# Performance work log

Measured on AMD Instinct MI355X. Metric: run time of the kernel, lower is better.

Reference implementation:

```python
import jax, jax.numpy as jnp
import numpy as np

SLOT_DIM = 128
HIDDEN = 64


def setup_inputs() -> dict:
    key = jax.random.key(0)
    k1, k2, k3, k4, k5 = jax.random.split(key, 5)
    b, k, d, h = 64, 128, SLOT_DIM, HIDDEN
    slots = jax.random.normal(k1, (b, k, d), dtype=jnp.float32)
    # edge_mlp params: Linear(2d -> h), Linear(h -> 1)
    s1 = 1.0 / np.sqrt(2 * d)
    W1 = jax.random.uniform(k2, (h, 2 * d), minval=-s1, maxval=s1, dtype=jnp.float32)
    b1 = jax.random.uniform(k3, (h,), minval=-s1, maxval=s1, dtype=jnp.float32)
    s2 = 1.0 / np.sqrt(h)
    W2 = jax.random.uniform(k4, (h,), minval=-s2, maxval=s2, dtype=jnp.float32)
    b2 = jax.random.uniform(k5, (), minval=-s2, maxval=s2, dtype=jnp.float32)
    return {"slots": slots, "W1": W1, "b1": b1, "W2": W2, "b2": b2}


def reference(slots, W1, b1, W2, b2):
    # slots: (b,k,d). Original concatenates [left,right] along features then
    # applies Linear(2d->h). Equivalent (same math): split W1 into halves and
    # broadcast-add, avoiding the (b,k,k,2d) concat tensor.
    b, k, d = slots.shape
    left_h = jnp.einsum('bkd,hd->bkh', slots, W1[:, :d])   # (b,k,h)
    right_h = jnp.einsum('bkd,hd->bkh', slots, W1[:, d:])  # (b,k,h)
    hidden = jax.nn.relu(left_h[:, :, None, :] + right_h[:, None, :, :] + b1)  # (b,k,k,h)
    logits = jnp.einsum('bijh,h->bij', hidden, W2) + b2    # (b,k,k)
    adj = jax.nn.sigmoid(logits)
    eye = jnp.eye(k, dtype=adj.dtype)[None]
    return adj * (1.0 - eye)
```

## Files before the change

kernel.cpp:

```cpp
#include <hip/hip_runtime.h>

#define BB 64
#define KK 128
#define DD 128

typedef __attribute__((ext_vector_type(8))) short bf16x8;
typedef __attribute__((ext_vector_type(4))) float f32x4;
typedef _Float16 half2v __attribute__((ext_vector_type(2)));
typedef __fp16 fp16x2 __attribute__((ext_vector_type(2)));

__device__ __forceinline__ unsigned cvt_pk_bf16(float x, float y) {
    unsigned r;
    asm("v_cvt_pk_bf16_f32 %0, %1, %2" : "=v"(r) : "v"(x), "v"(y));
    return r;
}

__device__ __forceinline__ unsigned cvt_pkrtz_u(float x, float y) {
    const fp16x2 pk = __builtin_amdgcn_cvt_pkrtz(x, y);
    return __builtin_bit_cast(unsigned, pk);
}

__device__ __forceinline__ unsigned pk_add_relu(unsigned a, unsigned b) {
    unsigned s, r;
    asm("v_pk_add_f16 %0, %1, %2" : "=v"(s) : "v"(a), "v"(b));
    asm("v_pk_max_f16 %0, %1, 0" : "=v"(r) : "v"(s));
    return r;
}

__device__ __forceinline__ float dot2acc(unsigned a, unsigned b, float c) {
#if __has_builtin(__builtin_amdgcn_fdot2)
    return __builtin_amdgcn_fdot2(__builtin_bit_cast(half2v, a),
                                  __builtin_bit_cast(half2v, b), c, false);
#else
    float r;
    asm("v_dot2_f32_f16 %0, %1, %2, %3" : "=v"(r) : "v"(a), "v"(b), "v"(c));
    return r;
#endif
}

__global__ __launch_bounds__(256, 2) void fused_kernel(
    const float* __restrict__ slots, const float* __restrict__ W1,
    const float* __restrict__ b1, const float* __restrict__ W2,
    const float* __restrict__ b2p, float* __restrict__ out)
{
    __shared__ unsigned smem_w[9632];
    char* smem = (char*)smem_w;

    const int t   = threadIdx.x;
    const int blk = blockIdx.x;
    const int b   = blk >> 3;
    const int it  = (blk >> 2) & 1;
    const int jt  = blk & 3;

    const int lane = t & 63;
    const int w    = t >> 6;
    const int lr   = lane & 15;
    const int lk   = lane >> 4;
    const int side = w >> 1;
    const int grp  = w & 1;

    const float b2 = *b2p;
    const float b1lo = (side == 0) ? b1[grp * 32 + lr]      : 0.0f;
    const float b1hi = (side == 0) ? b1[grp * 32 + 16 + lr] : 0.0f;
    float w2lo = 0.f, w2hi = 0.f;
    if (t < 32) {
        const int hl = (t & 15) + 32 * (t >> 4);
        w2lo = W2[hl]; w2hi = W2[hl + 16];
    }

    bf16x8 bfr[2][4];
#pragma unroll
    for (int n = 0; n < 2; ++n)
#pragma unroll
        for (int kf = 0; kf < 4; ++kf) {
            const int rowB = grp * 32 + n * 16 + lr;
            const float* p = W1 + rowB * 256 + side * 128 + kf * 32 + lk * 8;
            const float4 f0 = *reinterpret_cast<const float4*>(p);
            const float4 f1 = *reinterpret_cast<const float4*>(p + 4);
            uint4 pk;
            pk.x = cvt_pk_bf16(f0.x, f0.y); pk.y = cvt_pk_bf16(f0.z, f0.w);
            pk.z = cvt_pk_bf16(f1.x, f1.y); pk.w = cvt_pk_bf16(f1.z, f1.w);
            bfr[n][kf] = __builtin_bit_cast(bf16x8, pk);
        }

    {
        const float* srcI = slots + ((size_t)(b * KK) + it * 64) * DD;
        const float* srcJ = slots + ((size_t)(b * KK) + jt * 32) * DD;
#pragma unroll
        for (int x0 = 0; x0 < 1536; x0 += 256) {
            const int x = x0 + t;
            const int row = x >> 4, cb = x & 15;
            const float* src = (row < 64 ? srcI + row * DD
                                         : srcJ + (row - 64) * DD) + cb * 8;
            const float4 f0 = *reinterpret_cast<const float4*>(src);
            const float4 f1 = *reinterpret_cast<const float4*>(src + 4);
            uint4 pk;
            pk.x = cvt_pk_bf16(f0.x, f0.y); pk.y = cvt_pk_bf16(f0.z, f0.w);
            pk.z = cvt_pk_bf16(f1.x, f1.y); pk.w = cvt_pk_bf16(f1.z, f1.w);
            *reinterpret_cast<uint4*>(smem + row * 256 + ((cb ^ (row & 7)) << 4)) = pk;
        }
    }
    __syncthreads();

    f32x4 acc[4][2];
#pragma unroll
    for (int m = 0; m < 4; ++m)
#pragma unroll
        for (int n = 0; n < 2; ++n) acc[m][n] = f32x4{0.f, 0.f, 0.f, 0.f};

#pragma unroll
    for (int m = 0; m < 4; ++m) {
        if (side == 1 && m >= 2) continue;
#pragma unroll
        for (int kf = 0; kf < 4; ++kf) {
            const int row = side * 64 + 16 * m + lr;
            const int cb  = kf * 4 + lk;
            const bf16x8 af = *reinterpret_cast<const bf16x8*>(
                smem + row * 256 + ((cb ^ (row & 7)) << 4));
#pragma unroll
            for (int n = 0; n < 2; ++n)
                acc[m][n] = __builtin_amdgcn_mfma_f32_16x16x32_bf16(
                    af, bfr[n][kf], acc[m][n], 0, 0, 0);
        }
    }

    {
        unsigned* dst = smem_w + (side ? 8448 : 6144);
#pragma unroll
        for (int m = 0; m < 4; ++m) {
            if (side == 1 && m >= 2) continue;
#pragma unroll
            for (int r = 0; r < 4; ++r) {
                const int row = 16 * m + 4 * lk + r;
                dst[row * 36 + grp * 16 + lr] =
                    cvt_pkrtz_u(acc[m][0][r] + b1lo, acc[m][1][r] + b1hi);
            }
        }
        if (t < 32) smem_w[9600 + t] = cvt_pkrtz_u(w2lo, w2hi);
    }
    __syncthreads();

    const int tx = t & 15;
    const int ty = t >> 4;
    const unsigned* LsP = smem_w + 6144;
    const unsigned* RsP = smem_w + 8448;
    const unsigned* W2p = smem_w + 9600;

    uint4 w2r[8];
#pragma unroll
    for (int s = 0; s < 8; ++s)
        w2r[s] = *reinterpret_cast<const uint4*>(W2p + s * 4);

    float pacc[4][2] = {};
    uint4 l4a[4], r4a[2], l4b[4], r4b[2];

#define LD_STEP(L4, R4, s)                                                        \
    {                                                                             \
        _Pragma("unroll") for (int ii = 0; ii < 4; ++ii)                          \
            L4[ii] = *reinterpret_cast<const uint4*>(LsP + (ty + 16 * ii) * 36 + (s) * 4); \
        _Pragma("unroll") for (int jj = 0; jj < 2; ++jj)                          \
            R4[jj] = *reinterpret_cast<const uint4*>(RsP + (tx + 16 * jj) * 36 + (s) * 4); \
    }

#define COMPUTE_STEP(L4, R4, s)                                                   \
    {                                                                             \
        _Pragma("unroll") for (int ii = 0; ii < 4; ++ii)                          \
        _Pragma("unroll") for (int jj = 0; jj < 2; ++jj) {                        \
            float a = pacc[ii][jj];                                               \
            a = dot2acc(pk_add_relu(L4[ii].x, R4[jj].x), w2r[s].x, a);            \
            a = dot2acc(pk_add_relu(L4[ii].y, R4[jj].y), w2r[s].y, a);            \
            a = dot2acc(pk_add_relu(L4[ii].z, R4[jj].z), w2r[s].z, a);            \
            a = dot2acc(pk_add_relu(L4[ii].w, R4[jj].w), w2r[s].w, a);            \
            pacc[ii][jj] = a;                                                     \
        }                                                                         \
    }

    LD_STEP(l4a, r4a, 0)
#pragma unroll
    for (int sp = 0; sp < 4; ++sp) {
        LD_STEP(l4b, r4b, 2 * sp + 1)
        COMPUTE_STEP(l4a, r4a, 2 * sp)
        if (sp < 3) LD_STEP(l4a, r4a, 2 * sp + 2)
        COMPUTE_STEP(l4b, r4b, 2 * sp + 1)
    }
#undef LD_STEP
#undef COMPUTE_STEP

#pragma unroll
    for (int ii = 0; ii < 4; ++ii) {
        const int gi = it * 64 + ty + 16 * ii;
        float* orow = out + ((size_t)(b * KK) + gi) * KK + jt * 32;
#pragma unroll
        for (int jj = 0; jj < 2; ++jj) {
            const int jl = tx + 16 * jj;
            const int gj = jt * 32 + jl;
            const float xv = pacc[ii][jj] + b2;
            const float sg = 1.0f / (1.0f + __expf(-xv));
            orow[jl] = (gi == gj) ? 0.0f : sg;
        }
    }
}

extern "C" void kernel_launch(void* const* d_in, const int* in_sizes, int n_in,
                              void* d_out, int out_size, void* d_ws, size_t ws_size,
                              hipStream_t stream) {
    const float* slots = (const float*)d_in[0];
    const float* W1    = (const float*)d_in[1];
    const float* b1    = (const float*)d_in[2];
    const float* W2    = (const float*)d_in[3];
    const float* b2    = (const float*)d_in[4];
    float* out = (float*)d_out;
    (void)d_ws; (void)ws_size; (void)in_sizes; (void)n_in; (void)out_size;

    fused_kernel<<<BB * 8, 256, 0, stream>>>(slots, W1, b1, W2, b2, out);
}
```

Before: 14.88 us.

## Use 64x64 output tiles, load MFMA operands directly from global, remap blocks per XCD

Output tiles per block grow from 64x32 to 64x64, halving the grid to 256 blocks and cutting the redundant per-block first-layer GEMM work relative to pairwise output. The slot rows are no longer staged through swizzled shared memory. Each wave loads and converts its A fragments straight from global memory, which removes a barrier and shrinks LDS use. Block indices are remapped so that the blocks of one batch land on the same XCD for L2 locality. In exchange, fewer blocks than CUs may leave parts of the GPU idle, and the pairwise stage needs more registers per thread.

```diff
diff --git a/kernel.cpp b/kernel.cpp
--- a/kernel.cpp
+++ b/kernel.cpp
@@ -38,19 +38,20 @@
 #endif
 }
 
-__global__ __launch_bounds__(256, 2) void fused_kernel(
+__global__ __launch_bounds__(256) void fused_kernel(
     const float* __restrict__ slots, const float* __restrict__ W1,
     const float* __restrict__ b1, const float* __restrict__ W2,
     const float* __restrict__ b2p, float* __restrict__ out)
 {
-    __shared__ unsigned smem_w[9632];
-    char* smem = (char*)smem_w;
-
-    const int t   = threadIdx.x;
-    const int blk = blockIdx.x;
-    const int b   = blk >> 3;
-    const int it  = (blk >> 2) & 1;
-    const int jt  = blk & 3;
+    __shared__ unsigned smem_w[4640];
+
+    const int t     = threadIdx.x;
+    const int blk   = blockIdx.x;
+    const int xcd   = blk & 7;
+    const int local = blk >> 3;
+    const int b     = xcd * 8 + (local >> 2);
+    const int it    = (local >> 1) & 1;
+    const int jt    = local & 1;
 
     const int lane = t & 63;
     const int w    = t >> 6;
@@ -59,13 +60,13 @@
     const int side = w >> 1;
     const int grp  = w & 1;
 
-    const float b2 = *b2p;
+    const float b2v  = *b2p;
     const float b1lo = (side == 0) ? b1[grp * 32 + lr]      : 0.0f;
     const float b1hi = (side == 0) ? b1[grp * 32 + 16 + lr] : 0.0f;
-    float w2lo = 0.f, w2hi = 0.f;
+
     if (t < 32) {
         const int hl = (t & 15) + 32 * (t >> 4);
-        w2lo = W2[hl]; w2hi = W2[hl + 16];
+        smem_w[4608 + t] = cvt_pkrtz_u(W2[hl], W2[hl + 16]);
     }
 
     bf16x8 bfr[2][4];
@@ -83,89 +84,74 @@
             bfr[n][kf] = __builtin_bit_cast(bf16x8, pk);
         }
 
-    {
-        const float* srcI = slots + ((size_t)(b * KK) + it * 64) * DD;
-        const float* srcJ = slots + ((size_t)(b * KK) + jt * 32) * DD;
-#pragma unroll
-        for (int x0 = 0; x0 < 1536; x0 += 256) {
-            const int x = x0 + t;
-            const int row = x >> 4, cb = x & 15;
-            const float* src = (row < 64 ? srcI + row * DD
-                                         : srcJ + (row - 64) * DD) + cb * 8;
-            const float4 f0 = *reinterpret_cast<const float4*>(src);
-            const float4 f1 = *reinterpret_cast<const float4*>(src + 4);
+    const int arow0 = (side == 0) ? it * 64 : jt * 64;
+    const float* abase = slots + ((size_t)(b * KK) + arow0) * DD;
+
+    f32x4 acc[4][2];
+#pragma unroll
+    for (int m = 0; m < 4; ++m)
+#pragma unroll
+        for (int n = 0; n < 2; ++n) acc[m][n] = f32x4{0.f, 0.f, 0.f, 0.f};
+
+#pragma unroll
+    for (int m = 0; m < 4; ++m) {
+        bf16x8 af[4];
+#pragma unroll
+        for (int kf = 0; kf < 4; ++kf) {
+            const float* p = abase + (m * 16 + lr) * DD + kf * 32 + lk * 8;
+            const float4 f0 = *reinterpret_cast<const float4*>(p);
+            const float4 f1 = *reinterpret_cast<const float4*>(p + 4);
             uint4 pk;
             pk.x = cvt_pk_bf16(f0.x, f0.y); pk.y = cvt_pk_bf16(f0.z, f0.w);
             pk.z = cvt_pk_bf16(f1.x, f1.y); pk.w = cvt_pk_bf16(f1.z, f1.w);
-            *reinterpret_cast<uint4*>(smem + row * 256 + ((cb ^ (row & 7)) << 4)) = pk;
-        }
-    }
-    __syncthreads();
-
-    f32x4 acc[4][2];
-#pragma unroll
-    for (int m = 0; m < 4; ++m)
-#pragma unroll
-        for (int n = 0; n < 2; ++n) acc[m][n] = f32x4{0.f, 0.f, 0.f, 0.f};
-
-#pragma unroll
-    for (int m = 0; m < 4; ++m) {
-        if (side == 1 && m >= 2) continue;
+            af[kf] = __builtin_bit_cast(bf16x8, pk);
+        }
 #pragma unroll
         for (int kf = 0; kf < 4; ++kf) {
-            const int row = side * 64 + 16 * m + lr;
-            const int cb  = kf * 4 + lk;
-            const bf16x8 af = *reinterpret_cast<const bf16x8*>(
-                smem + row * 256 + ((cb ^ (row & 7)) << 4));
-#pragma unroll
-            for (int n = 0; n < 2; ++n)
-                acc[m][n] = __builtin_amdgcn_mfma_f32_16x16x32_bf16(
-                    af, bfr[n][kf], acc[m][n], 0, 0, 0);
+            acc[m][0] = __builtin_amdgcn_mfma_f32_16x16x32_bf16(af[kf], bfr[0][kf], acc[m][0], 0, 0, 0);
+            acc[m][1] = __builtin_amdgcn_mfma_f32_16x16x32_bf16(af[kf], bfr[1][kf], acc[m][1], 0, 0, 0);
         }
     }
 
     {
-        unsigned* dst = smem_w + (side ? 8448 : 6144);
-#pragma unroll
-        for (int m = 0; m < 4; ++m) {
-            if (side == 1 && m >= 2) continue;
+        unsigned* dst = smem_w + (side ? 2304 : 0);
+#pragma unroll
+        for (int m = 0; m < 4; ++m)
 #pragma unroll
             for (int r = 0; r < 4; ++r) {
                 const int row = 16 * m + 4 * lk + r;
                 dst[row * 36 + grp * 16 + lr] =
                     cvt_pkrtz_u(acc[m][0][r] + b1lo, acc[m][1][r] + b1hi);
             }
-        }
-        if (t < 32) smem_w[9600 + t] = cvt_pkrtz_u(w2lo, w2hi);
     }
     __syncthreads();
 
     const int tx = t & 15;
     const int ty = t >> 4;
-    const unsigned* LsP = smem_w + 6144;
-    const unsigned* RsP = smem_w + 8448;
-    const unsigned* W2p = smem_w + 9600;
+    const unsigned* LsP = smem_w;
+    const unsigned* RsP = smem_w + 2304;
+    const unsigned* W2p = smem_w + 4608;
 
     uint4 w2r[8];
 #pragma unroll
     for (int s = 0; s < 8; ++s)
         w2r[s] = *reinterpret_cast<const uint4*>(W2p + s * 4);
 
-    float pacc[4][2] = {};
-    uint4 l4a[4], r4a[2], l4b[4], r4b[2];
+    float pacc[4][4] = {};
+    uint4 l4a[4], r4a[4], l4b[4], r4b[4];
 
 #define LD_STEP(L4, R4, s)                                                        \
     {                                                                             \
         _Pragma("unroll") for (int ii = 0; ii < 4; ++ii)                          \
             L4[ii] = *reinterpret_cast<const uint4*>(LsP + (ty + 16 * ii) * 36 + (s) * 4); \
-        _Pragma("unroll") for (int jj = 0; jj < 2; ++jj)                          \
+        _Pragma("unroll") for (int jj = 0; jj < 4; ++jj)                          \
             R4[jj] = *reinterpret_cast<const uint4*>(RsP + (tx + 16 * jj) * 36 + (s) * 4); \
     }
 
 #define COMPUTE_STEP(L4, R4, s)                                                   \
     {                                                                             \
         _Pragma("unroll") for (int ii = 0; ii < 4; ++ii)                          \
-        _Pragma("unroll") for (int jj = 0; jj < 2; ++jj) {                        \
+        _Pragma("unroll") for (int jj = 0; jj < 4; ++jj) {                        \
             float a = pacc[ii][jj];                                               \
             a = dot2acc(pk_add_relu(L4[ii].x, R4[jj].x), w2r[s].x, a);            \
             a = dot2acc(pk_add_relu(L4[ii].y, R4[jj].y), w2r[s].y, a);            \
@@ -189,12 +175,12 @@
 #pragma unroll
     for (int ii = 0; ii < 4; ++ii) {
         const int gi = it * 64 + ty + 16 * ii;
-        float* orow = out + ((size_t)(b * KK) + gi) * KK + jt * 32;
-#pragma unroll
-        for (int jj = 0; jj < 2; ++jj) {
+        float* orow = out + ((size_t)(b * KK) + gi) * KK + jt * 64;
+#pragma unroll
+        for (int jj = 0; jj < 4; ++jj) {
             const int jl = tx + 16 * jj;
-            const int gj = jt * 32 + jl;
-            const float xv = pacc[ii][jj] + b2;
+            const int gj = jt * 64 + jl;
+            const float xv = pacc[ii][jj] + b2v;
             const float sg = 1.0f / (1.0f + __expf(-xv));
             orow[jl] = (gi == gj) ? 0.0f : sg;
         }
@@ -212,5 +198,5 @@
     float* out = (float*)d_out;
     (void)d_ws; (void)ws_size; (void)in_sizes; (void)n_in; (void)out_size;
 
-    fused_kernel<<<BB * 8, 256, 0, stream>>>(slots, W1, b1, W2, b2, out);
-}
+    fused_kernel<<<BB * 4, 256, 0, stream>>>(slots, W1, b1, W2, b2, out);
+}
```

Measured after the change: 17.75 us. 1.19x slower.
